# Optimization experiments

Hardware: AMD Instinct MI355X
Metric: run time of the kernel (lower is better)

Reference implementation:

```python
import jax, jax.numpy as jnp
import numpy as np

LOG2 = 0.6931471805599453

def logcosh(x):
    # numerically stable log(cosh(x)) = |x| + log1p(exp(-2|x|)) - log(2)
    ax = jnp.abs(x)
    return ax + jnp.log1p(jnp.exp(-2.0 * ax)) - LOG2

def setup_inputs() -> dict:
    key = jax.random.key(0)
    k1, k2, k3 = jax.random.split(key, 3)
    B, N, G, F = 16384, 1024, 256, 16  # batch, n_sites, n_symm, alpha_symm
    # each row of perms is a valid permutation of [0, N)
    perms = jax.vmap(lambda k: jax.random.permutation(k, N))(jax.random.split(k1, G)).astype(jnp.int32)
    x = jax.random.normal(k2, (B, N), dtype=jnp.float32)
    W = jax.random.normal(k3, (N, F), dtype=jnp.float32) * 0.1  # kernel_init = normal(0.1)
    b = jnp.zeros((F,), dtype=jnp.float32)
    v_bias = jnp.zeros((1,), dtype=jnp.float32)
    return {"x": x, "W": W, "b": b, "v_bias": v_bias, "perms": perms}

def reference(x, W, b, v_bias, perms):
    # scan over group permutations: gather x by perm, matmul, bias, logcosh, sum
    def f(carry, perm):
        y = x[..., perm] @ W + b          # [B, F]
        return carry + jnp.sum(logcosh(y), axis=-1), None
    y0 = jnp.zeros(x.shape[:-1], dtype=x.dtype)
    y_out, _ = jax.lax.scan(f, y0, perms)
    y_out = y_out + v_bias[0] * jnp.sum(x, axis=-1)
    return y_out
```

## Files before the change

### kernel.cpp

```cpp
#include <hip/hip_runtime.h>
#include <math.h>

typedef __bf16 bf16x8 __attribute__((ext_vector_type(8)));
typedef float f32x4 __attribute__((ext_vector_type(4)));


__device__ __forceinline__ unsigned short f2bf(float f) {
    unsigned int u = __float_as_uint(f);
    u += 0x7FFFu + ((u >> 16) & 1u);
    return (unsigned short)(u >> 16);
}

__device__ __forceinline__ float logcosh_fast(float v) {
    float a = fabsf(v);
    float t = __expf(-2.0f * a);
    return a + (__logf(1.0f + t) - 0.6931471805599453f);
}

template <int CTRL>
__device__ __forceinline__ float dppadd(float x) {
    int y = __builtin_amdgcn_update_dpp(0, __float_as_int(x), CTRL, 0xf, 0xf, true);
    return x + __int_as_float(y);
}

__device__ __forceinline__ void gload_lds16(const void* g, void* l) {
    __builtin_amdgcn_global_load_lds(
        (__attribute__((address_space(1))) void*)(void*)g,
        (__attribute__((address_space(3))) void*)l, 16, 0, 0);
}

__global__ __launch_bounds__(256) void k_invert(const int* __restrict__ perms,
                                                int* __restrict__ inv) {
    int t = blockIdx.x * 256 + threadIdx.x;
    int g = t >> 10, n = t & 1023;
    inv[(g << 10) + perms[t]] = n;
}

__global__ __launch_bounds__(256) void k_build_bt(const float* __restrict__ W,
                                                  const int* __restrict__ inv,
                                                  unsigned short* __restrict__ bT) {
    int j = blockIdx.x;
    int g = j >> 4, f = j & 15;
    const int* invg = inv + (g << 10);
    size_t rowbase = (size_t)j << 10;
#pragma unroll
    for (int i = 0; i < 4; ++i) {
        int k = (i << 8) + threadIdx.x;
        int n = invg[k];
        bT[rowbase + k] = f2bf(W[(n << 4) + f]);
    }
}

__global__ __launch_bounds__(256) void k_convert(const float* __restrict__ x,
                                                 const float* __restrict__ vb,
                                                 unsigned short* __restrict__ xb,
                                                 float* __restrict__ out) {
    int row = blockIdx.x, tid = threadIdx.x;
    size_t base = ((size_t)row << 10) + (tid << 2);
    float4 v = *reinterpret_cast<const float4*>(x + base);
    ushort4 h;
    h.x = f2bf(v.x); h.y = f2bf(v.y); h.z = f2bf(v.z); h.w = f2bf(v.w);
    *reinterpret_cast<ushort4*>(xb + base) = h;
    float s = v.x + v.y + v.z + v.w;
#pragma unroll
    for (int off = 32; off > 0; off >>= 1) s += __shfl_down(s, off);
    __shared__ float ls[4];
    if ((tid & 63) == 0) ls[tid >> 6] = s;
    __syncthreads();
    if (tid == 0) out[row] = vb[0] * (ls[0] + ls[1] + ls[2] + ls[3]);
}

__global__ __launch_bounds__(256) void k_gemm(const unsigned short* __restrict__ xb,
                                              const unsigned short* __restrict__ bT,
                                              const float* __restrict__ bias,
                                              float* __restrict__ partial, int B) {
    __shared__ unsigned short As[128 * 64];
    __shared__ unsigned short Bs[128 * 64];
    __shared__ float rowsum2[2][128];

    const int tid = threadIdx.x;
    const int lane = tid & 63;
    const int wv = tid >> 6;
    const int wrow = wv >> 1, wcol = wv & 1;
    const int cbx = blockIdx.x;
    const int row0 = blockIdx.y << 7;
    const int j0 = cbx << 7;

    const int lr = lane & 15;
    const int lk = lane >> 4;

    f32x4 acc[4][4];
#pragma unroll
    for (int m = 0; m < 4; ++m)
#pragma unroll
        for (int n = 0; n < 4; ++n)
            acc[m][n] = {0.f, 0.f, 0.f, 0.f};

    for (int kt = 0; kt < 1024; kt += 64) {
#pragma unroll
        for (int i = 0; i < 4; ++i) {
            int c0 = i * 256 + wv * 64;
            int chunk = c0 + lane;
            int r = chunk >> 3;
            int cs = (chunk & 7) ^ (r & 7);
            gload_lds16(xb + (((size_t)(row0 + r)) << 10) + kt + (cs << 3),
                        As + (c0 << 3));
        }
#pragma unroll
        for (int i = 0; i < 4; ++i) {
            int c0 = i * 256 + wv * 64;
            int chunk = c0 + lane;
            int r = chunk >> 3;
            int cs = (chunk & 7) ^ (r & 7);
            gload_lds16(bT + (((size_t)(j0 + r)) << 10) + kt + (cs << 3),
                        Bs + (c0 << 3));
        }
        __syncthreads();

#pragma unroll
        for (int kk = 0; kk < 2; ++kk) {
            bf16x8 aF[4], bF[4];
#pragma unroll
            for (int m = 0; m < 4; ++m) {
                int r = (wrow << 6) + (m << 4) + lr;
                int pos = ((kk << 2) + lk) ^ (r & 7);
                aF[m] = *reinterpret_cast<const bf16x8*>(As + (r << 6) + (pos << 3));
            }
#pragma unroll
            for (int n = 0; n < 4; ++n) {
                int r = (wcol << 6) + (n << 4) + lr;
                int pos = ((kk << 2) + lk) ^ (r & 7);
                bF[n] = *reinterpret_cast<const bf16x8*>(Bs + (r << 6) + (pos << 3));
            }
#pragma unroll
            for (int m = 0; m < 4; ++m)
#pragma unroll
                for (int n = 0; n < 4; ++n)
                    acc[m][n] = __builtin_amdgcn_mfma_f32_16x16x32_bf16(
                        aF[m], bF[n], acc[m][n], 0, 0, 0);
        }
        __syncthreads();
    }

    const float bv = bias[lr];
#pragma unroll
    for (int m = 0; m < 4; ++m) {
#pragma unroll
        for (int r = 0; r < 4; ++r) {
            float s = 0.f;
#pragma unroll
            for (int n = 0; n < 4; ++n) s += logcosh_fast(acc[m][n][r] + bv);
            s = dppadd<0x111>(s);
            s = dppadd<0x112>(s);
            s = dppadd<0x114>(s);
            s = dppadd<0x118>(s);
            if (lr == 15)
                rowsum2[wcol][(wrow << 6) + (m << 4) + (lk << 2) + r] = s;
        }
    }
    __syncthreads();
    if (tid < 128)
        partial[(size_t)cbx * B + row0 + tid] = rowsum2[0][tid] + rowsum2[1][tid];
}

__global__ __launch_bounds__(256) void k_final(const float* __restrict__ partial,
                                               float* __restrict__ out, int ncb, int B) {
    int b = blockIdx.x * 256 + threadIdx.x;
    float s = out[b];
    for (int c = 0; c < ncb; ++c) s += partial[(size_t)c * B + b];
    out[b] = s;
}

extern "C" void kernel_launch(void* const* d_in, const int* in_sizes, int n_in,
                              void* d_out, int out_size, void* d_ws, size_t ws_size,
                              hipStream_t stream) {
    const float* x      = (const float*)d_in[0];
    const float* W      = (const float*)d_in[1];
    const float* bias   = (const float*)d_in[2];
    const float* v_bias = (const float*)d_in[3];
    const int*   perms  = (const int*)d_in[4];
    float* out = (float*)d_out;

    const int N  = 1024;
    const int B  = in_sizes[0] / N;
    const int G  = in_sizes[4] / N;
    const int GF = G * 16;
    const int NCB = GF / 128;

    char* w = (char*)d_ws;
    unsigned short* xb = (unsigned short*)w;
    unsigned short* bT = (unsigned short*)(w + (size_t)B * N * 2);
    int* inv = (int*)(w + (size_t)B * N * 2 + (size_t)GF * N * 2);
    float* partial = (float*)(w + (size_t)B * N * 2 + (size_t)GF * N * 2
                              + (size_t)G * N * 4);

    k_invert<<<G * N / 256, 256, 0, stream>>>(perms, inv);
    k_build_bt<<<GF, 256, 0, stream>>>(W, inv, bT);
    k_convert<<<B, 256, 0, stream>>>(x, v_bias, xb, out);
    k_gemm<<<dim3(NCB, B / 128), 256, 0, stream>>>(xb, bT, bias, partial, B);
    k_final<<<B / 256, 256, 0, stream>>>(partial, out, NCB, B);
}
```

Before: 224.0 us.

## Rewrite GEMM as 256x256 tile with double-buffered LDS and interleaved staging

The GEMM kernel moves from 128x128 tiles with 4 waves to 256x256 tiles with 8 waves. LDS is double-buffered, and the next tile's global-to-LDS loads are split into quarters and interleaved with four MFMA sub-blocks. Explicit waitcnt, sched_barrier and setprio control the overlap, and an XCD-aware block swizzle is added. The aim is to hide memory latency and raise arithmetic intensity, at the cost of more registers and LDS per block (64KB) and fewer blocks, which may lower occupancy.

After: 196.7 us. -12.2%, faster.

```diff
diff --git a/kernel.cpp b/kernel.cpp
--- a/kernel.cpp
+++ b/kernel.cpp
@@ -70,81 +70,151 @@
     if (tid == 0) out[row] = vb[0] * (ls[0] + ls[1] + ls[2] + ls[3]);
 }
 
-__global__ __launch_bounds__(256) void k_gemm(const unsigned short* __restrict__ xb,
+
+#define MFMA_QUAD(MH, NH)                                                        \
+    _Pragma("unroll") for (int m_ = 0; m_ < 4; ++m_)                             \
+    _Pragma("unroll") for (int n_ = 0; n_ < 2; ++n_)                             \
+    _Pragma("unroll") for (int kk_ = 0; kk_ < 2; ++kk_)                          \
+        acc[(MH) * 4 + m_][(NH) * 2 + n_] =                                      \
+            __builtin_amdgcn_mfma_f32_16x16x32_bf16(                             \
+                aF[(MH) * 4 + m_][kk_], bF[(NH) * 2 + n_][kk_],                  \
+                acc[(MH) * 4 + m_][(NH) * 2 + n_], 0, 0, 0);
+
+__global__ __launch_bounds__(512) void k_gemm(const unsigned short* __restrict__ xb,
                                               const unsigned short* __restrict__ bT,
                                               const float* __restrict__ bias,
                                               float* __restrict__ partial, int B) {
-    __shared__ unsigned short As[128 * 64];
-    __shared__ unsigned short Bs[128 * 64];
-    __shared__ float rowsum2[2][128];
+    __shared__ unsigned short As[2][256 * 64];
+    __shared__ unsigned short Bs[2][256 * 64];
 
     const int tid = threadIdx.x;
     const int lane = tid & 63;
     const int wv = tid >> 6;
-    const int wrow = wv >> 1, wcol = wv & 1;
-    const int cbx = blockIdx.x;
-    const int row0 = blockIdx.y << 7;
-    const int j0 = cbx << 7;
-
+    const int wm = wv >> 2;
+    const int wn = wv & 3;
     const int lr = lane & 15;
     const int lk = lane >> 4;
 
-    f32x4 acc[4][4];
-#pragma unroll
-    for (int m = 0; m < 4; ++m)
+    const int fid = blockIdx.y * gridDim.x + blockIdx.x;
+    const int cpx = (gridDim.x * gridDim.y) >> 3;
+    const int swz = (fid & 7) * cpx + (fid >> 3);
+    const int cbx = swz & 15;
+    const int row0 = (swz >> 4) << 8;
+    const int j0 = cbx << 8;
+
+    const unsigned short* xbase = xb + ((size_t)row0 << 10);
+    const unsigned short* bbase = bT + ((size_t)j0 << 10);
+
+    auto stage_half = [&](unsigned short* dst, const unsigned short* src, int h) {
+#pragma unroll
+        for (int j = 0; j < 2; ++j) {
+            int c0 = (h * 128 + j * 64) * 8;
+            int cc = c0 + tid;
+            int r = cc >> 3;
+            int cs = (cc & 7) ^ (r & 7);
+            gload_lds16(src + (((size_t)r) << 10) + (cs << 3),
+                        dst + ((c0 + wv * 64) << 3));
+        }
+    };
+    auto stage_s = [&](int t, int s) {
+        int tt = (s == 0) ? t + 1 : t + 2;
+        if (tt >= 16) return;
+        int p = tt & 1;
+        int kt = tt << 6;
+        if (s == 0)      stage_half(Bs[p], bbase + kt, 1);
+        else if (s == 1) stage_half(As[p], xbase + kt, 0);
+        else if (s == 2) stage_half(As[p], xbase + kt, 1);
+        else             stage_half(Bs[p], bbase + kt, 0);
+    };
+
+    f32x4 acc[8][4];
+#pragma unroll
+    for (int m = 0; m < 8; ++m)
 #pragma unroll
         for (int n = 0; n < 4; ++n)
             acc[m][n] = {0.f, 0.f, 0.f, 0.f};
 
-    for (int kt = 0; kt < 1024; kt += 64) {
-#pragma unroll
-        for (int i = 0; i < 4; ++i) {
-            int c0 = i * 256 + wv * 64;
-            int chunk = c0 + lane;
-            int r = chunk >> 3;
-            int cs = (chunk & 7) ^ (r & 7);
-            gload_lds16(xb + (((size_t)(row0 + r)) << 10) + kt + (cs << 3),
-                        As + (c0 << 3));
-        }
-#pragma unroll
-        for (int i = 0; i < 4; ++i) {
-            int c0 = i * 256 + wv * 64;
-            int chunk = c0 + lane;
-            int r = chunk >> 3;
-            int cs = (chunk & 7) ^ (r & 7);
-            gload_lds16(bT + (((size_t)(j0 + r)) << 10) + kt + (cs << 3),
-                        Bs + (c0 << 3));
-        }
-        __syncthreads();
-
-#pragma unroll
-        for (int kk = 0; kk < 2; ++kk) {
-            bf16x8 aF[4], bF[4];
-#pragma unroll
-            for (int m = 0; m < 4; ++m) {
-                int r = (wrow << 6) + (m << 4) + lr;
+    stage_half(As[0], xbase + 0, 0);
+    stage_half(As[0], xbase + 0, 1);
+    stage_half(Bs[0], bbase + 0, 0);
+    stage_half(Bs[0], bbase + 0, 1);
+    stage_half(As[1], xbase + 64, 0);
+    stage_half(As[1], xbase + 64, 1);
+    stage_half(Bs[1], bbase + 64, 0);
+    asm volatile("s_waitcnt vmcnt(6)" ::: "memory");
+    __builtin_amdgcn_s_barrier();
+
+#pragma unroll 2
+    for (int t = 0; t < 16; ++t) {
+        const int p = t & 1;
+        const unsigned short* Ap = As[p];
+        const unsigned short* Bp = Bs[p];
+        bf16x8 aF[8][2], bF[4][2];
+
+        __builtin_amdgcn_sched_barrier(0);
+#pragma unroll
+        for (int m = 0; m < 8; ++m) {
+            int r = wm * 128 + m * 16 + lr;
+#pragma unroll
+            for (int kk = 0; kk < 2; ++kk) {
                 int pos = ((kk << 2) + lk) ^ (r & 7);
-                aF[m] = *reinterpret_cast<const bf16x8*>(As + (r << 6) + (pos << 3));
+                aF[m][kk] = *reinterpret_cast<const bf16x8*>(Ap + (r << 6) + (pos << 3));
             }
-#pragma unroll
-            for (int n = 0; n < 4; ++n) {
-                int r = (wcol << 6) + (n << 4) + lr;
-                int pos = ((kk << 2) + lk) ^ (r & 7);
-                bF[n] = *reinterpret_cast<const bf16x8*>(Bs + (r << 6) + (pos << 3));
+        }
+#pragma unroll
+        for (int n = 0; n < 4; ++n) {
+            int rb = wn * 64 + n * 16 + lr;
+#pragma unroll
+            for (int kk = 0; kk < 2; ++kk) {
+                int pos = ((kk << 2) + lk) ^ (rb & 7);
+                bF[n][kk] = *reinterpret_cast<const bf16x8*>(Bp + (rb << 6) + (pos << 3));
             }
-#pragma unroll
-            for (int m = 0; m < 4; ++m)
-#pragma unroll
-                for (int n = 0; n < 4; ++n)
-                    acc[m][n] = __builtin_amdgcn_mfma_f32_16x16x32_bf16(
-                        aF[m], bF[n], acc[m][n], 0, 0, 0);
-        }
-        __syncthreads();
-    }
-
+        }
+        stage_s(t, 0);
+        asm volatile("s_waitcnt lgkmcnt(0)" ::: "memory");
+        __builtin_amdgcn_sched_barrier(0);
+        __builtin_amdgcn_s_setprio(1);
+        MFMA_QUAD(0, 0)
+        __builtin_amdgcn_s_setprio(0);
+        __builtin_amdgcn_s_barrier();
+
+        __builtin_amdgcn_sched_barrier(0);
+        stage_s(t, 1);
+        __builtin_amdgcn_s_barrier();
+        __builtin_amdgcn_sched_barrier(0);
+        __builtin_amdgcn_s_setprio(1);
+        MFMA_QUAD(1, 0)
+        __builtin_amdgcn_s_setprio(0);
+        __builtin_amdgcn_s_barrier();
+
+        __builtin_amdgcn_sched_barrier(0);
+        stage_s(t, 2);
+        __builtin_amdgcn_s_barrier();
+        __builtin_amdgcn_sched_barrier(0);
+        __builtin_amdgcn_s_setprio(1);
+        MFMA_QUAD(0, 1)
+        __builtin_amdgcn_s_setprio(0);
+        __builtin_amdgcn_s_barrier();
+
+        __builtin_amdgcn_sched_barrier(0);
+        stage_s(t, 3);
+        __builtin_amdgcn_s_barrier();
+        __builtin_amdgcn_sched_barrier(0);
+        __builtin_amdgcn_s_setprio(1);
+        MFMA_QUAD(1, 1)
+        __builtin_amdgcn_s_setprio(0);
+        if (t < 14) {
+            asm volatile("s_waitcnt vmcnt(6)" ::: "memory");
+        } else if (t == 14) {
+            asm volatile("s_waitcnt vmcnt(0)" ::: "memory");
+        }
+        __builtin_amdgcn_s_barrier();
+    }
+
+    float* rowsum = (float*)&As[0][0];
     const float bv = bias[lr];
 #pragma unroll
-    for (int m = 0; m < 4; ++m) {
+    for (int m = 0; m < 8; ++m) {
 #pragma unroll
         for (int r = 0; r < 4; ++r) {
             float s = 0.f;
@@ -155,12 +225,14 @@
             s = dppadd<0x114>(s);
             s = dppadd<0x118>(s);
             if (lr == 15)
-                rowsum2[wcol][(wrow << 6) + (m << 4) + (lk << 2) + r] = s;
+                rowsum[wn * 256 + wm * 128 + m * 16 + lk * 4 + r] = s;
         }
     }
     __syncthreads();
-    if (tid < 128)
-        partial[(size_t)cbx * B + row0 + tid] = rowsum2[0][tid] + rowsum2[1][tid];
+    if (tid < 256) {
+        float s = rowsum[tid] + rowsum[256 + tid] + rowsum[512 + tid] + rowsum[768 + tid];
+        partial[(size_t)cbx * B + row0 + tid] = s;
+    }
 }
 
 __global__ __launch_bounds__(256) void k_final(const float* __restrict__ partial,
@@ -185,7 +257,7 @@
     const int B  = in_sizes[0] / N;
     const int G  = in_sizes[4] / N;
     const int GF = G * 16;
-    const int NCB = GF / 128;
+    const int NCB = GF / 256;
 
     char* w = (char*)d_ws;
     unsigned short* xb = (unsigned short*)w;
@@ -197,6 +269,6 @@
     k_invert<<<G * N / 256, 256, 0, stream>>>(perms, inv);
     k_build_bt<<<GF, 256, 0, stream>>>(W, inv, bT);
     k_convert<<<B, 256, 0, stream>>>(x, v_bias, xb, out);
-    k_gemm<<<dim3(NCB, B / 128), 256, 0, stream>>>(xb, bT, bias, partial, B);
+    k_gemm<<<dim3(NCB, B / 256), 512, 0, stream>>>(xb, bT, bias, partial, B);
     k_final<<<B / 256, 256, 0, stream>>>(partial, out, NCB, B);
 }
```

## Double-buffer B tiles in LDS and load A fragments directly from global

Applied to the files above, without the earlier changes.

The GEMM main loop now double-buffers only the B tile in LDS and reads the A operand fragments straight from global memory into registers, prefetching one k-tile ahead. Explicit vmcnt/lgkmcnt waits, sched barriers, raw s_barrier and setprio are meant to overlap loads with MFMA work and drop one of the two barriers per iteration. A block-index swizzle changes tile ordering for L2 reuse, and launch bounds request two blocks per CU. The manual waitcnt accounting is fragile, and uncoalesced A loads from global may cost bandwidth.

Result: slower. 333.5 us (+48.9%).

```diff
diff --git a/kernel.cpp b/kernel.cpp
--- a/kernel.cpp
+++ b/kernel.cpp
@@ -28,6 +28,16 @@
         (__attribute__((address_space(1))) void*)(void*)g,
         (__attribute__((address_space(3))) void*)l, 16, 0, 0);
 }
+
+template <int N>
+__device__ __forceinline__ void vmwait() {
+    if constexpr (N == 0)       asm volatile("s_waitcnt vmcnt(0)" ::: "memory");
+    else if constexpr (N == 8)  asm volatile("s_waitcnt vmcnt(8)" ::: "memory");
+    else if constexpr (N == 12) asm volatile("s_waitcnt vmcnt(12)" ::: "memory");
+}
+
+#define SBAR()  __builtin_amdgcn_s_barrier()
+#define SCHED() __builtin_amdgcn_sched_barrier(0)
 
 __global__ __launch_bounds__(256) void k_invert(const int* __restrict__ perms,
                                                 int* __restrict__ inv) {
@@ -70,25 +80,91 @@
     if (tid == 0) out[row] = vb[0] * (ls[0] + ls[1] + ls[2] + ls[3]);
 }
 
-__global__ __launch_bounds__(256) void k_gemm(const unsigned short* __restrict__ xb,
-                                              const unsigned short* __restrict__ bT,
-                                              const float* __restrict__ bias,
-                                              float* __restrict__ partial, int B) {
-    __shared__ unsigned short As[128 * 64];
-    __shared__ unsigned short Bs[128 * 64];
-    __shared__ float rowsum2[2][128];
+
+template <bool STB, bool ISSA, int VMA, int VME>
+__device__ __forceinline__ void tile_gemm(
+    const unsigned short* __restrict__ Bp,
+    unsigned short* __restrict__ Bdst,
+    const unsigned short* __restrict__ bsrc,
+    const unsigned short* __restrict__ xsrc,
+    bf16x8 (&aFu)[4][2], bf16x8 (&aFl)[4][2], f32x4 (&acc)[4][4],
+    int aoff, int bRow, int po0, int po1, int tid, int wv) {
+    if (STB) {
+#pragma unroll
+        for (int i = 0; i < 4; ++i) {
+            int c0 = i * 256 + wv * 64;
+            int cc = i * 256 + tid;
+            int r = cc >> 3;
+            int cs = (cc & 7) ^ (r & 7);
+            gload_lds16(bsrc + (r << 10) + (cs << 3), Bdst + (c0 << 3));
+        }
+    }
+    SCHED();
+    if (ISSA) {
+#pragma unroll
+        for (int m = 0; m < 4; ++m) {
+#pragma unroll
+            for (int kk = 0; kk < 2; ++kk)
+                aFl[m][kk] = *reinterpret_cast<const bf16x8*>(
+                    xsrc + aoff + m * 16384 + kk * 32);
+        }
+    }
+    SCHED();
+    bf16x8 bF[4][2];
+#pragma unroll
+    for (int n = 0; n < 4; ++n) {
+        bF[n][0] = *reinterpret_cast<const bf16x8*>(Bp + bRow + po0 + n * 1024);
+        bF[n][1] = *reinterpret_cast<const bf16x8*>(Bp + bRow + po1 + n * 1024);
+    }
+    SCHED();
+    vmwait<VMA>();
+    asm volatile("s_waitcnt lgkmcnt(0)" ::: "memory");
+    SCHED();
+    __builtin_amdgcn_s_setprio(1);
+#pragma unroll
+    for (int m = 0; m < 4; ++m)
+#pragma unroll
+        for (int n = 0; n < 4; ++n)
+#pragma unroll
+            for (int kk = 0; kk < 2; ++kk)
+                acc[m][n] = __builtin_amdgcn_mfma_f32_16x16x32_bf16(
+                    aFu[m][kk], bF[n][kk], acc[m][n], 0, 0, 0);
+    __builtin_amdgcn_s_setprio(0);
+    SCHED();
+    if (VME >= 0) vmwait<VME>();
+    SBAR();
+}
+
+__global__ __launch_bounds__(256, 2) void k_gemm(const unsigned short* __restrict__ xb,
+                                                 const unsigned short* __restrict__ bT,
+                                                 const float* __restrict__ bias,
+                                                 float* __restrict__ partial, int B) {
+    __shared__ unsigned short Bs[2][128 * 64];
 
     const int tid = threadIdx.x;
     const int lane = tid & 63;
     const int wv = tid >> 6;
-    const int wrow = wv >> 1, wcol = wv & 1;
-    const int cbx = blockIdx.x;
-    const int row0 = blockIdx.y << 7;
-    const int j0 = cbx << 7;
-
+    const int wm = wv >> 1;
+    const int wn = wv & 1;
     const int lr = lane & 15;
     const int lk = lane >> 4;
 
+    const int fid = blockIdx.y * gridDim.x + blockIdx.x;
+    const int cpx = (gridDim.x * gridDim.y) >> 3;
+    const int swz = (fid & 7) * cpx + (fid >> 3);
+    const int rowb = swz & 127;
+    const int cbx = swz >> 7;
+    const int row0 = rowb << 7;
+    const int j0 = cbx << 7;
+
+    const unsigned short* xbase = xb + ((size_t)row0 << 10);
+    const unsigned short* bbase = bT + ((size_t)j0 << 10);
+
+    const int aoff = (wm * 64 + lr) * 1024 + lk * 8;
+    const int bRow = (wn * 64 + lr) * 64;
+    const int po0 = (lk ^ (lr & 7)) * 8;
+    const int po1 = ((4 + lk) ^ (lr & 7)) * 8;
+
     f32x4 acc[4][4];
 #pragma unroll
     for (int m = 0; m < 4; ++m)
@@ -96,52 +172,49 @@
         for (int n = 0; n < 4; ++n)
             acc[m][n] = {0.f, 0.f, 0.f, 0.f};
 
-    for (int kt = 0; kt < 1024; kt += 64) {
-#pragma unroll
-        for (int i = 0; i < 4; ++i) {
-            int c0 = i * 256 + wv * 64;
-            int chunk = c0 + lane;
-            int r = chunk >> 3;
-            int cs = (chunk & 7) ^ (r & 7);
-            gload_lds16(xb + (((size_t)(row0 + r)) << 10) + kt + (cs << 3),
-                        As + (c0 << 3));
-        }
-#pragma unroll
-        for (int i = 0; i < 4; ++i) {
-            int c0 = i * 256 + wv * 64;
-            int chunk = c0 + lane;
-            int r = chunk >> 3;
-            int cs = (chunk & 7) ^ (r & 7);
-            gload_lds16(bT + (((size_t)(j0 + r)) << 10) + kt + (cs << 3),
-                        Bs + (c0 << 3));
-        }
-        __syncthreads();
-
-#pragma unroll
-        for (int kk = 0; kk < 2; ++kk) {
-            bf16x8 aF[4], bF[4];
-#pragma unroll
-            for (int m = 0; m < 4; ++m) {
-                int r = (wrow << 6) + (m << 4) + lr;
-                int pos = ((kk << 2) + lk) ^ (r & 7);
-                aF[m] = *reinterpret_cast<const bf16x8*>(As + (r << 6) + (pos << 3));
-            }
-#pragma unroll
-            for (int n = 0; n < 4; ++n) {
-                int r = (wcol << 6) + (n << 4) + lr;
-                int pos = ((kk << 2) + lk) ^ (r & 7);
-                bF[n] = *reinterpret_cast<const bf16x8*>(Bs + (r << 6) + (pos << 3));
-            }
-#pragma unroll
-            for (int m = 0; m < 4; ++m)
-#pragma unroll
-                for (int n = 0; n < 4; ++n)
-                    acc[m][n] = __builtin_amdgcn_mfma_f32_16x16x32_bf16(
-                        aF[m], bF[n], acc[m][n], 0, 0, 0);
-        }
-        __syncthreads();
-    }
-
+    bf16x8 aF0[4][2], aF1[4][2];
+
+#pragma unroll
+    for (int i = 0; i < 4; ++i) {
+        int c0 = i * 256 + wv * 64;
+        int cc = i * 256 + tid;
+        int r = cc >> 3;
+        int cs = (cc & 7) ^ (r & 7);
+        gload_lds16(bbase + (r << 10) + (cs << 3), &Bs[0][0] + (c0 << 3));
+    }
+#pragma unroll
+    for (int i = 0; i < 4; ++i) {
+        int c0 = i * 256 + wv * 64;
+        int cc = i * 256 + tid;
+        int r = cc >> 3;
+        int cs = (cc & 7) ^ (r & 7);
+        gload_lds16(bbase + 64 + (r << 10) + (cs << 3), &Bs[1][0] + (c0 << 3));
+    }
+    SCHED();
+#pragma unroll
+    for (int m = 0; m < 4; ++m)
+#pragma unroll
+        for (int kk = 0; kk < 2; ++kk)
+            aF0[m][kk] = *reinterpret_cast<const bf16x8*>(xbase + aoff + m * 16384 + kk * 32);
+    SCHED();
+    vmwait<8>();
+    SBAR();
+
+    tile_gemm<false, true, 8, -1>(&Bs[0][0], &Bs[1][0], bbase, xbase + 64,
+                                  aF0, aF1, acc, aoff, bRow, po0, po1, tid, wv);
+    for (int tt = 0; tt < 7; ++tt) {
+        const int t0 = tt * 2;
+        tile_gemm<true, true, 12, 8>(&Bs[1][0], &Bs[0][0],
+                                     bbase + ((t0 + 2) << 6), xbase + ((t0 + 2) << 6),
+                                     aF1, aF0, acc, aoff, bRow, po0, po1, tid, wv);
+        tile_gemm<true, true, 12, 8>(&Bs[0][0], &Bs[1][0],
+                                     bbase + ((t0 + 3) << 6), xbase + ((t0 + 3) << 6),
+                                     aF0, aF1, acc, aoff, bRow, po0, po1, tid, wv);
+    }
+    tile_gemm<false, false, 0, -1>(&Bs[1][0], &Bs[0][0], bbase, xbase,
+                                   aF1, aF0, acc, aoff, bRow, po0, po1, tid, wv);
+
+    float* rowsum = (float*)&Bs[0][0];
     const float bv = bias[lr];
 #pragma unroll
     for (int m = 0; m < 4; ++m) {
@@ -155,12 +228,12 @@
             s = dppadd<0x114>(s);
             s = dppadd<0x118>(s);
             if (lr == 15)
-                rowsum2[wcol][(wrow << 6) + (m << 4) + (lk << 2) + r] = s;
+                rowsum[wn * 128 + wm * 64 + m * 16 + lk * 4 + r] = s;
         }
     }
     __syncthreads();
     if (tid < 128)
-        partial[(size_t)cbx * B + row0 + tid] = rowsum2[0][tid] + rowsum2[1][tid];
+        partial[(size_t)cbx * B + row0 + tid] = rowsum[tid] + rowsum[128 + tid];
 }
 
 __global__ __launch_bounds__(256) void k_final(const float* __restrict__ partial,
```
